# Kernel optimization log

Hardware: AMD Instinct MI355X
Metric: run time of the kernel (lower is better)

Reference implementation:

```python
import jax, jax.numpy as jnp
import numpy as np

# static config (matches init_kwargs / input_specs)
B, S, D, H, DH = 4, 2048, 2048, 16, 128
MAX_LEN = 1024  # round_up_to_multiple_of_256(max ragged length); lengths below max at 1024
ROPE_BASE = 10000.0


def setup_inputs() -> dict:
    key = jax.random.key(0)
    ks = jax.random.split(key, 8)
    q_src = jax.random.normal(ks[0], (B, MAX_LEN, D), jnp.float32)
    k_src = jax.random.normal(ks[1], (B, S, D), jnp.float32)
    v_src = jax.random.normal(ks[2], (B, S, D), jnp.float32)
    std = 1.0 / np.sqrt(D)
    Wq = jax.random.normal(ks[3], (D, H * DH), jnp.float32) * std
    Wk = jax.random.normal(ks[4], (D, H * DH), jnp.float32) * std
    Wv = jax.random.normal(ks[5], (D, H * DH), jnp.float32) * std
    Wo = jax.random.normal(ks[6], (H * DH, D), jnp.float32) * (1.0 / np.sqrt(H * DH))
    # mask[0]: causal bool [B,S,S]; mask[1]: full position ids [B,S]
    mask0 = jnp.broadcast_to(jnp.tril(jnp.ones((S, S), bool)), (B, S, S))
    pos_full = jnp.broadcast_to(jnp.arange(S, dtype=jnp.int32), (B, S))
    # ragged skip_mask: row i keeps lengths[i] random positions (max 1024 -> MAX_LEN)
    lengths = jnp.array([1024, 896, 768, 640], jnp.int32)
    scores = jax.random.uniform(ks[7], (B, S))
    ranks = jnp.argsort(jnp.argsort(scores, axis=1), axis=1)
    skip_mask = ranks < lengths[:, None]
    return {"q_src": q_src, "k_src": k_src, "v_src": v_src,
            "Wq": Wq, "Wk": Wk, "Wv": Wv, "Wo": Wo,
            "mask0": mask0, "pos_full": pos_full, "skip_mask": skip_mask}


def _rope(x, positions):
    # x: [B,H,L,DH], positions: [B,L] int -> rotary embedding on full head dim
    dh = x.shape[-1]
    inv_freq = 1.0 / (ROPE_BASE ** (jnp.arange(0, dh, 2, dtype=jnp.float32) / dh))
    freqs = positions.astype(jnp.float32)[:, :, None] * inv_freq      # [B,L,dh/2]
    emb = jnp.concatenate([freqs, freqs], axis=-1)[:, None]           # [B,1,L,dh]
    x1, x2 = jnp.split(x, 2, axis=-1)
    rot = jnp.concatenate([-x2, x1], axis=-1)                         # rotate_half
    return x * jnp.cos(emb) + rot * jnp.sin(emb)


def reference(q_src, k_src, v_src, Wq, Wk, Wv, Wo, mask0, pos_full, skip_mask):
    def heads(x, W):
        y = x @ W
        return y.reshape(x.shape[0], x.shape[1], H, DH).transpose(0, 2, 1, 3)

    q = heads(q_src, Wq)   # [B,H,MAX_LEN,DH]
    k = heads(k_src, Wk)   # [B,H,S,DH]
    v = heads(v_src, Wv)   # [B,H,S,DH]

    # _trim_attention_mask: gather kept rows (True-first, stable order), pad to MAX_LEN
    order = jnp.argsort(jnp.where(skip_mask, 0, 1), axis=1)[:, :MAX_LEN]  # [B,MAX_LEN]
    n = skip_mask.sum(axis=1)                                             # ragged lengths
    valid = jnp.arange(MAX_LEN)[None, :] < n[:, None]                     # [B,MAX_LEN]
    amask = jnp.take_along_axis(mask0, order[:, :, None], axis=1) & valid[:, :, None]
    pos_trim = jnp.where(valid, jnp.take_along_axis(pos_full, order, axis=1), 0)

    # RoPE: trimmed positions for q, full positions for k
    q = _rope(q, pos_trim)
    k = _rope(k, pos_full)

    # masked SDPA; fully-masked (padded) query rows -> zero output
    logits = jnp.einsum('bhld,bhsd->bhls', q, k) / np.sqrt(DH).astype(np.float32)
    logits = jnp.where(amask[:, None], logits, jnp.finfo(logits.dtype).min)
    probs = jax.nn.softmax(logits, axis=-1) * valid[:, None, :, None]
    ctx = jnp.einsum('bhls,bhsd->bhld', probs, v)                         # [B,H,MAX_LEN,DH]

    out = ctx.transpose(0, 2, 1, 3).reshape(B, MAX_LEN, H * DH) @ Wo     # [B,MAX_LEN,D]
    return out
```

## Files before the change

kernel.cpp:

```cpp
#include <hip/hip_runtime.h>

#define BB 4
#define SS 2048
#define DD 2048
#define HH 16
#define DHD 128
#define MAXL 1024

typedef __bf16 bf16x8 __attribute__((ext_vector_type(8)));
typedef float f32x4 __attribute__((ext_vector_type(4)));
typedef unsigned int u32_as1 __attribute__((address_space(1)));
typedef unsigned int u32_as3 __attribute__((address_space(3)));

__device__ __forceinline__ unsigned short f2bf(float f) {
  unsigned int u = __builtin_bit_cast(unsigned int, f);
  u += 0x7fffu + ((u >> 16) & 1u);
  return (unsigned short)(u >> 16);
}
__device__ __forceinline__ float bf2f(unsigned short h) {
  unsigned int u = ((unsigned int)h) << 16;
  return __builtin_bit_cast(float, u);
}
union U4 { uint4 u; bf16x8 b; };
__device__ __forceinline__ bf16x8 ldfrag(const unsigned short* p) {
  U4 x; x.u = *(const uint4*)p; return x.b;
}
__device__ __forceinline__ void gl_lds16(const void* g, void* l) {
  __builtin_amdgcn_global_load_lds((const u32_as1*)g, (u32_as3*)l, 16, 0, 0);
}

template <int C>
__device__ __forceinline__ float dppf(float x) {
  return __builtin_bit_cast(float,
      __builtin_amdgcn_mov_dpp(__builtin_bit_cast(int, x), C, 0xF, 0xF, true));
}
__device__ __forceinline__ float rmax16(float x) {
  x = fmaxf(x, dppf<0xB1>(x));
  x = fmaxf(x, dppf<0x4E>(x));
  x = fmaxf(x, dppf<0x141>(x));
  x = fmaxf(x, dppf<0x140>(x));
  return x;
}
__device__ __forceinline__ float radd16(float x) {
  x += dppf<0xB1>(x);
  x += dppf<0x4E>(x);
  x += dppf<0x141>(x);
  x += dppf<0x140>(x);
  return x;
}

__global__ void build_pos(const int* __restrict__ skip, int* __restrict__ posk,
                          int* __restrict__ nval) {
  int b = blockIdx.x, t = threadIdx.x;
  __shared__ int cnts[64], offs[64];
  const int* row = skip + b * SS;
  int c = 0;
  for (int i = 0; i < 32; i++) c += (row[t * 32 + i] != 0);
  cnts[t] = c;
  __syncthreads();
  if (t == 0) {
    int run = 0;
    for (int i = 0; i < 64; i++) { offs[i] = run; run += cnts[i]; }
    nval[b] = run > MAXL ? MAXL : run;
  }
  __syncthreads();
  int o = offs[t];
  for (int i = 0; i < 32; i++)
    if (row[t * 32 + i]) { if (o < MAXL) posk[b * MAXL + o] = t * 32 + i; o++; }
  int nb = nval[b];
  for (int l = nb + t; l < MAXL; l += 64) posk[b * MAXL + l] = -1;
}

__global__ __launch_bounds__(256) void cvt3(const float* __restrict__ q,
                                            const float* __restrict__ k,
                                            const float* __restrict__ v,
                                            unsigned short* __restrict__ oq,
                                            unsigned short* __restrict__ ok,
                                            unsigned short* __restrict__ ov) {
  const int nq = BB * MAXL * DD / 4, nk = BB * SS * DD / 4;
  int idx = blockIdx.x * 256 + threadIdx.x;
  const float* src; unsigned short* dst; int off;
  if (idx < nq) { src = q; dst = oq; off = idx; }
  else if (idx < nq + nk) { src = k; dst = ok; off = idx - nq; }
  else { src = v; dst = ov; off = idx - nq - nk; }
  float4 vv = ((const float4*)src)[off];
  ushort4 h;
  h.x = f2bf(vv.x); h.y = f2bf(vv.y); h.z = f2bf(vv.z); h.w = f2bf(vv.w);
  ((ushort4*)dst)[off] = h;
}

__global__ __launch_bounds__(256) void transpose_w4(const float* __restrict__ w0,
    const float* __restrict__ w1, const float* __restrict__ w2, const float* __restrict__ w3,
    unsigned short* __restrict__ o0, unsigned short* __restrict__ o1,
    unsigned short* __restrict__ o2, unsigned short* __restrict__ o3) {
  __shared__ __align__(16) unsigned short tile[64 * 76];
  const float* W; unsigned short* Wt;
  switch (blockIdx.z) {
    case 0: W = w0; Wt = o0; break;
    case 1: W = w1; Wt = o1; break;
    case 2: W = w2; Wt = o2; break;
    default: W = w3; Wt = o3; break;
  }
  int tx = threadIdx.x;
  int K0 = blockIdx.y * 64, N0 = blockIdx.x * 64;
  #pragma unroll
  for (int i = 0; i < 4; i++) {
    int r = (tx >> 4) + i * 16, c4 = (tx & 15) * 4;
    float4 v = *(const float4*)&W[(size_t)(K0 + r) * DD + N0 + c4];
    ushort4 h;
    h.x = f2bf(v.x); h.y = f2bf(v.y); h.z = f2bf(v.z); h.w = f2bf(v.w);
    *(ushort4*)&tile[r * 76 + c4] = h;
  }
  __syncthreads();
  #pragma unroll
  for (int i = 0; i < 4; i++) {
    int n = (tx >> 4) + i * 16, k4 = (tx & 15) * 4;
    ushort4 h;
    h.x = tile[(k4 + 0) * 76 + n];
    h.y = tile[(k4 + 1) * 76 + n];
    h.z = tile[(k4 + 2) * 76 + n];
    h.w = tile[(k4 + 3) * 76 + n];
    *(ushort4*)&Wt[(size_t)(N0 + n) * DD + K0 + k4] = h;
  }
}

template <int BM>
__global__ __launch_bounds__(512, 2) void gemm8(const unsigned short* __restrict__ A,
                                                const unsigned short* __restrict__ Bt,
                                                void* __restrict__ Cp,
                                                int M, int N, int K, int mode, int Lbits) {
  constexpr int AW = BM * 64;
  __shared__ __align__(16) unsigned short lds[(BM + 256) * 64 * 2];
  unsigned short* const Abuf = lds;
  unsigned short* const Bbuf = lds + 2 * AW;

  const int tid = threadIdx.x;
  const int lane = tid & 63, quad = lane >> 4, c = lane & 15;
  const int w = tid >> 6;
  const int wm = (w >> 2) * (BM / 2), wn = (w & 3) * 64;

  const int nwg = gridDim.x * gridDim.y;
  const int bid0 = blockIdx.y * gridDim.x + blockIdx.x;
  const int cpx = nwg >> 3;
  const int bid = (bid0 & 7) * cpx + (bid0 >> 3);
  const int bx = bid % gridDim.x;
  const int by = bid / gridDim.x;
  const size_t tm = (size_t)by * BM, tn = (size_t)bx * 256;

  constexpr int MR = BM / 32;
  f32x4 acc[MR][4] = {};

  const int trow = tid >> 3;
  const int tch = ((tid & 7) ^ (trow & 7)) * 8;
  const unsigned short* gA = A + (tm + trow) * (size_t)K + tch;
  const unsigned short* gB = Bt + (tn + trow) * (size_t)K + tch;
  constexpr int ALD = BM / 64;
  constexpr int NLD = ALD + 4;

  auto STAGE = [&](int sel, int kk) {
    unsigned short* ad = Abuf + sel * AW;
    unsigned short* bd = Bbuf + sel * 16384;
    #pragma unroll
    for (int i = 0; i < ALD; i++)
      gl_lds16(gA + kk + (size_t)(i * 64) * K, ad + i * 4096 + tid * 8);
    #pragma unroll
    for (int i = 0; i < 4; i++)
      gl_lds16(gB + kk + (size_t)(i * 64) * K, bd + i * 4096 + tid * 8);
  };

  const int nkt = K >> 6;
  STAGE(0, 0);

  for (int t = 0; t < nkt; ++t) {
    const int sel = t & 1;
    const unsigned short* as = Abuf + sel * AW;
    const unsigned short* bs = Bbuf + sel * 16384;
    if (t + 1 < nkt) {
      STAGE(sel ^ 1, (t + 1) << 6);
      asm volatile("s_waitcnt vmcnt(%0)" ::"i"(NLD) : "memory");
    } else {
      asm volatile("s_waitcnt vmcnt(0)" ::: "memory");
    }
    __builtin_amdgcn_s_barrier();

    bf16x8 a0[4][2], b01[2][2], b23[2][2];
    #pragma unroll
    for (int i = 0; i < 4; i++)
      #pragma unroll
      for (int ks = 0; ks < 2; ks++)
        a0[i][ks] = ldfrag(&as[(wm + i * 16 + c) * 64 + (((ks * 4 + quad) ^ (c & 7)) << 3)]);
    #pragma unroll
    for (int j = 0; j < 2; j++)
      #pragma unroll
      for (int ks = 0; ks < 2; ks++)
        b01[j][ks] = ldfrag(&bs[(wn + j * 16 + c) * 64 + (((ks * 4 + quad) ^ (c & 7)) << 3)]);
    __builtin_amdgcn_s_barrier();
    __builtin_amdgcn_s_setprio(1);
    #pragma unroll
    for (int i = 0; i < 4; i++)
      #pragma unroll
      for (int j = 0; j < 2; j++)
        #pragma unroll
        for (int ks = 0; ks < 2; ks++)
          acc[i][j] = __builtin_amdgcn_mfma_f32_16x16x32_bf16(a0[i][ks], b01[j][ks], acc[i][j], 0, 0, 0);
    __builtin_amdgcn_s_setprio(0);
    __builtin_amdgcn_s_barrier();
    #pragma unroll
    for (int j = 0; j < 2; j++)
      #pragma unroll
      for (int ks = 0; ks < 2; ks++)
        b23[j][ks] = ldfrag(&bs[(wn + 32 + j * 16 + c) * 64 + (((ks * 4 + quad) ^ (c & 7)) << 3)]);
    __builtin_amdgcn_s_barrier();
    __builtin_amdgcn_s_setprio(1);
    #pragma unroll
    for (int i = 0; i < 4; i++)
      #pragma unroll
      for (int j = 0; j < 2; j++)
        #pragma unroll
        for (int ks = 0; ks < 2; ks++)
          acc[i][2 + j] = __builtin_amdgcn_mfma_f32_16x16x32_bf16(a0[i][ks], b23[j][ks], acc[i][2 + j], 0, 0, 0);
    __builtin_amdgcn_s_setprio(0);
    __builtin_amdgcn_s_barrier();

    if constexpr (BM == 256) {
      bf16x8 a1[4][2];
      #pragma unroll
      for (int i = 0; i < 4; i++)
        #pragma unroll
        for (int ks = 0; ks < 2; ks++)
          a1[i][ks] = ldfrag(&as[(wm + 64 + i * 16 + c) * 64 + (((ks * 4 + quad) ^ (c & 7)) << 3)]);
      __builtin_amdgcn_s_barrier();
      __builtin_amdgcn_s_setprio(1);
      #pragma unroll
      for (int i = 0; i < 4; i++)
        #pragma unroll
        for (int j = 0; j < 2; j++)
          #pragma unroll
          for (int ks = 0; ks < 2; ks++)
            acc[4 + i][j] = __builtin_amdgcn_mfma_f32_16x16x32_bf16(a1[i][ks], b01[j][ks], acc[4 + i][j], 0, 0, 0);
      __builtin_amdgcn_s_setprio(0);
      __builtin_amdgcn_s_barrier();
      __builtin_amdgcn_s_setprio(1);
      #pragma unroll
      for (int i = 0; i < 4; i++)
        #pragma unroll
        for (int j = 0; j < 2; j++)
          #pragma unroll
          for (int ks = 0; ks < 2; ks++)
            acc[4 + i][2 + j] = __builtin_amdgcn_mfma_f32_16x16x32_bf16(a1[i][ks], b23[j][ks], acc[4 + i][2 + j], 0, 0, 0);
      __builtin_amdgcn_s_setprio(0);
      __builtin_amdgcn_s_barrier();
    }
  }

  if (mode == 1) {
    float* Cf = (float*)Cp;
    #pragma unroll
    for (int i = 0; i < MR; i++)
      #pragma unroll
      for (int j = 0; j < 4; j++)
        #pragma unroll
        for (int r = 0; r < 4; r++) {
          size_t m = tm + wm + i * 16 + quad * 4 + r;
          size_t n = tn + wn + j * 16 + c;
          Cf[m * N + n] = acc[i][j][r];
        }
    return;
  }
  unsigned short* Cb = (unsigned short*)Cp;
  unsigned short* ep = lds + w * 4352;
  constexpr int MH = BM / 128;
  if (mode == 0) {
    const size_t Lmask = ((size_t)1 << Lbits) - 1;
    #pragma unroll
    for (int mh = 0; mh < MH; mh++) {
      #pragma unroll
      for (int i = 0; i < 4; i++)
        #pragma unroll
        for (int j = 0; j < 4; j++)
          #pragma unroll
          for (int r = 0; r < 4; r++)
            ep[(i * 16 + quad * 4 + r) * 68 + j * 16 + c] = f2bf(acc[mh * 4 + i][j][r]);
      #pragma unroll
      for (int it = 0; it < 8; it++) {
        int chunk = it * 64 + lane;
        int ml = chunk >> 3, nc = (chunk & 7) * 8;
        uint4 val = *(const uint4*)&ep[ml * 68 + nc];
        size_t m = tm + wm + mh * 64 + ml, n = tn + wn + nc;
        size_t b = m >> Lbits, l = m & Lmask, h = n >> 7, d = n & 127;
        *(uint4*)&Cb[(((b * HH + h) << Lbits) + l) * 128 + d] = val;
      }
    }
  } else {
    #pragma unroll
    for (int mh = 0; mh < MH; mh++) {
      #pragma unroll
      for (int i = 0; i < 4; i++)
        #pragma unroll
        for (int j = 0; j < 4; j++)
          #pragma unroll
          for (int r = 0; r < 4; r++)
            ep[(j * 16 + c) * 68 + i * 16 + quad * 4 + r] = f2bf(acc[mh * 4 + i][j][r]);
      #pragma unroll
      for (int it = 0; it < 8; it++) {
        int chunk = it * 64 + lane;
        int nl = chunk >> 3, mc = (chunk & 7) * 8;
        uint4 val = *(const uint4*)&ep[nl * 68 + mc];
        size_t n = tn + wn + nl, m = tm + wm + mh * 64 + mc;
        size_t b = m >> 11, s = m & 2047, h = n >> 7, d = n & 127;
        *(uint4*)&Cb[((b * HH + h) * 128 + d) * SS + s] = val;
      }
    }
  }
}

__global__ __launch_bounds__(256) void rope2(unsigned short* __restrict__ xq,
                                             unsigned short* __restrict__ xk,
                                             const int* __restrict__ posk) {
  const int Nq = BB * HH * MAXL * 64;
  int gid = blockIdx.x * 256 + threadIdx.x;
  unsigned short* x; int Lbits, idx, use_posk;
  if (gid < Nq) { x = xq; Lbits = 10; use_posk = 1; idx = gid; }
  else { x = xk; Lbits = 11; use_posk = 0; idx = gid - Nq; }
  int d = idx & 63;
  int rest = idx >> 6;
  int l = rest & ((1 << Lbits) - 1);
  int bh = rest >> Lbits;
  int b = bh >> 4;
  int p = use_posk ? posk[(b << 10) + l] : l;
  float ang = (float)p * __expf(-(float)d * 0.14391156831212787f);
  float sn, cs;
  __sincosf(ang, &sn, &cs);
  size_t base = (size_t)rest * 128;
  float x1 = bf2f(x[base + d]), x2 = bf2f(x[base + d + 64]);
  x[base + d]      = f2bf(x1 * cs - x2 * sn);
  x[base + d + 64] = f2bf(x2 * cs + x1 * sn);
}

__global__ __launch_bounds__(256) void attn_kernel(const unsigned short* __restrict__ qp,
                                                   const unsigned short* __restrict__ kp,
                                                   const unsigned short* __restrict__ vtp,
                                                   const int* __restrict__ posk,
                                                   const int* __restrict__ nval,
                                                   unsigned short* __restrict__ ctx) {
  __shared__ __align__(16) unsigned short k_s[2][64 * 128];
  __shared__ __align__(16) unsigned short vt_s[2][128 * 64];
  __shared__ __align__(16) unsigned short p_s[4 * 16 * 72];
  __shared__ int km_s[64];

  const int tid = threadIdx.x;
  const int w = tid >> 6, lane = tid & 63, quad = lane >> 4, c = lane & 15;
  const int bh = blockIdx.x, b = bh >> 4, h = bh & 15;
  const int qbase = blockIdx.y * 64;
  const int nb = nval[b];

  if (tid < 64) {
    int l = qbase + tid;
    km_s[tid] = (l < nb) ? posk[(b << 10) + l] : -1;
  }
  __syncthreads();

  const unsigned short* qg = qp + (((size_t)bh << 10) + qbase) * 128;
  bf16x8 aq[4];
  #pragma unroll
  for (int ks = 0; ks < 4; ks++)
    aq[ks] = ldfrag(&qg[(size_t)(w * 16 + c) * 128 + ks * 32 + quad * 8]);

  int lv = nb - 1 - qbase; lv = lv > 63 ? 63 : lv;
  const int tile_kmax = (lv >= 0) ? km_s[lv] : -1;
  const int nkt = (tile_kmax >= 0) ? ((tile_kmax >> 6) + 1) : 0;

  int wl = w * 16 + 15; if (wl > lv) wl = lv;
  const int wkmax = (wl >= w * 16) ? km_s[wl] : -1;

  int km[4];
  #pragma unroll
  for (int r = 0; r < 4; r++) km[r] = km_s[w * 16 + quad * 4 + r];

  const int srow = tid >> 4;
  const int kswz = (tid & 15) ^ (srow & 7);
  const unsigned short* kgp = kp + ((size_t)bh << 11) * 128 + (size_t)srow * 128 + kswz * 8;
  const int dvrow = tid >> 3;
  const int vswz = (tid & 7) ^ (dvrow & 7);
  const unsigned short* vgp = vtp + ((size_t)bh * 128 + dvrow) * SS + vswz * 8;

  auto STG = [&](int buf, int kb) {
    #pragma unroll
    for (int i = 0; i < 4; i++)
      gl_lds16(kgp + ((size_t)kb + i * 16) * 128, &k_s[buf][(i * 256 + tid) * 8]);
    #pragma unroll
    for (int i = 0; i < 4; i++)
      gl_lds16(vgp + (size_t)kb + (size_t)i * 32 * SS, &vt_s[buf][(i * 256 + tid) * 8]);
  };

  float m_i[4], l_i[4];
  #pragma unroll
  for (int r = 0; r < 4; r++) { m_i[r] = -1e30f; l_i[r] = 0.f; }
  f32x4 o[8];
  #pragma unroll
  for (int dj = 0; dj < 8; dj++) o[dj] = (f32x4){0.f, 0.f, 0.f, 0.f};

  if (nkt > 0) STG(0, 0);

  for (int kt = 0; kt < nkt; kt++) {
    const int cur = kt & 1;
    const int kb = kt * 64;
    if (kt + 1 < nkt) {
      STG(cur ^ 1, kb + 64);
      asm volatile("s_waitcnt vmcnt(8)" ::: "memory");
    } else {
      asm volatile("s_waitcnt vmcnt(0)" ::: "memory");
    }
    __builtin_amdgcn_s_barrier();

    if (kb <= wkmax) {
      f32x4 sa[4];
      #pragma unroll
      for (int j = 0; j < 4; j++) {
        sa[j] = (f32x4){0.f, 0.f, 0.f, 0.f};
        #pragma unroll
        for (int ks = 0; ks < 4; ks++) {
          bf16x8 bk = ldfrag(&k_s[cur][((j * 16 + c) << 7) + (((ks * 4 + quad) ^ (c & 7)) << 3)]);
          sa[j] = __builtin_amdgcn_mfma_f32_16x16x32_bf16(aq[ks], bk, sa[j], 0, 0, 0);
        }
      }

      const float scale = 0.08838834764831843f;
      float mt[4] = {-1e30f, -1e30f, -1e30f, -1e30f};
      #pragma unroll
      for (int j = 0; j < 4; j++) {
        int key = kb + j * 16 + c;
        #pragma unroll
        for (int r = 0; r < 4; r++) {
          float v = (key <= km[r]) ? sa[j][r] * scale : -1e30f;
          sa[j][r] = v;
          mt[r] = fmaxf(mt[r], v);
        }
      }
      float al[4], rs[4];
      #pragma unroll
      for (int r = 0; r < 4; r++) {
        mt[r] = rmax16(mt[r]);
        float mn = fmaxf(m_i[r], mt[r]);
        al[r] = __expf(m_i[r] - mn);
        m_i[r] = mn;
        rs[r] = 0.f;
      }
      #pragma unroll
      for (int j = 0; j < 4; j++)
        #pragma unroll
        for (int r = 0; r < 4; r++) {
          float pv = __expf(sa[j][r] - m_i[r]);
          sa[j][r] = pv;
          rs[r] += pv;
        }
      #pragma unroll
      for (int r = 0; r < 4; r++) {
        rs[r] = radd16(rs[r]);
        l_i[r] = l_i[r] * al[r] + rs[r];
      }
      #pragma unroll
      for (int dj = 0; dj < 8; dj++)
        #pragma unroll
        for (int r = 0; r < 4; r++) o[dj][r] *= al[r];

      #pragma unroll
      for (int j = 0; j < 4; j++)
        #pragma unroll
        for (int r = 0; r < 4; r++)
          p_s[w * 1152 + (quad * 4 + r) * 72 + j * 16 + c] = f2bf(sa[j][r]);

      #pragma unroll
      for (int ks2 = 0; ks2 < 2; ks2++) {
        bf16x8 ap = ldfrag(&p_s[w * 1152 + c * 72 + ks2 * 32 + quad * 8]);
        #pragma unroll
        for (int dj = 0; dj < 8; dj++) {
          bf16x8 bv = ldfrag(&vt_s[cur][((dj * 16 + c) << 6) + (((ks2 * 4 + quad) ^ (c & 7)) << 3)]);
          o[dj] = __builtin_amdgcn_mfma_f32_16x16x32_bf16(ap, bv, o[dj], 0, 0, 0);
        }
      }
    }
    __builtin_amdgcn_s_barrier();
  }

  #pragma unroll
  for (int r = 0; r < 4; r++) {
    int l = qbase + w * 16 + quad * 4 + r;
    bool ok = (l < nb);
    float inv = ok ? (1.0f / l_i[r]) : 0.0f;
    #pragma unroll
    for (int dj = 0; dj < 8; dj++)
      ctx[(((size_t)b << 10) + l) * (size_t)DD + h * 128 + dj * 16 + c] =
          f2bf(ok ? o[dj][r] * inv : 0.0f);
  }
}

extern "C" void kernel_launch(void* const* d_in, const int* in_sizes, int n_in,
                              void* d_out, int out_size, void* d_ws, size_t ws_size,
                              hipStream_t stream) {
  const float* q_src = (const float*)d_in[0];
  const float* k_src = (const float*)d_in[1];
  const float* v_src = (const float*)d_in[2];
  const float* Wq = (const float*)d_in[3];
  const float* Wk = (const float*)d_in[4];
  const float* Wv = (const float*)d_in[5];
  const float* Wo = (const float*)d_in[6];
  const int* skip = (const int*)d_in[9];

  char* p = (char*)d_ws;
  auto alloc = [&](size_t bytes) -> char* {
    char* r = p;
    p += (bytes + 255) & ~(size_t)255;
    return r;
  };
  unsigned short* a_q  = (unsigned short*)alloc((size_t)BB * MAXL * DD * 2);
  unsigned short* a_k  = (unsigned short*)alloc((size_t)BB * SS * DD * 2);
  unsigned short* a_v  = (unsigned short*)alloc((size_t)BB * SS * DD * 2);
  unsigned short* wt_q = (unsigned short*)alloc((size_t)DD * DD * 2);
  unsigned short* wt_k = (unsigned short*)alloc((size_t)DD * DD * 2);
  unsigned short* wt_v = (unsigned short*)alloc((size_t)DD * DD * 2);
  unsigned short* wt_o = (unsigned short*)alloc((size_t)DD * DD * 2);
  unsigned short* q_pro = (unsigned short*)alloc((size_t)BB * HH * MAXL * DHD * 2);
  unsigned short* k_pro = (unsigned short*)alloc((size_t)BB * HH * SS * DHD * 2);
  unsigned short* v_t   = (unsigned short*)alloc((size_t)BB * HH * SS * DHD * 2);
  int* posk = (int*)alloc((size_t)BB * MAXL * 4);
  int* nval = (int*)alloc(64);
  unsigned short* ctx = a_q;

  build_pos<<<BB, 64, 0, stream>>>(skip, posk, nval);
  cvt3<<<(BB * MAXL * DD + 2 * BB * SS * DD) / (4 * 256), 256, 0, stream>>>(
      q_src, k_src, v_src, a_q, a_k, a_v);
  transpose_w4<<<dim3(32, 32, 4), 256, 0, stream>>>(Wq, Wk, Wv, Wo, wt_q, wt_k, wt_v, wt_o);

  gemm8<128><<<dim3(8, 32), 512, 0, stream>>>(a_q, wt_q, q_pro, BB * MAXL, DD, DD, 0, 10);
  gemm8<256><<<dim3(8, 32), 512, 0, stream>>>(a_k, wt_k, k_pro, BB * SS, DD, DD, 0, 11);
  gemm8<256><<<dim3(8, 32), 512, 0, stream>>>(a_v, wt_v, v_t, BB * SS, DD, DD, 2, 11);

  rope2<<<(BB * HH * (MAXL + SS) * 64) / 256, 256, 0, stream>>>(q_pro, k_pro, posk);

  attn_kernel<<<dim3(BB * HH, MAXL / 64), 256, 0, stream>>>(q_pro, k_pro, v_t, posk, nval, ctx);

  gemm8<128><<<dim3(8, 32), 512, 0, stream>>>(ctx, wt_o, d_out, BB * MAXL, DD, DD, 1, 0);
}
```

Measured before the change: 692.7 us.

## Use fragment-major LDS layout, split K/V staging, fold scale and log2e into Q

The GEMM and attention kernels now store tiles in LDS in a fragment-major order, so each lane reads its MFMA fragment at lane*8 with no XOR swizzle arithmetic. The attention kernel moves from double-buffered K/V to single buffers with separate K and V prefetches placed between compute phases. This cuts LDS use, and launch bounds now request 4 blocks per CU. The softmax scale and log2e are folded into Q during RoPE so exp2 can be used directly. Masking is skipped for tiles that lie entirely below the causal limit. Single buffering with extra barriers may expose load latency, and the bf16 rounding of the prescaled Q changes slightly.

```diff
diff --git a/kernel.cpp b/kernel.cpp
--- a/kernel.cpp
+++ b/kernel.cpp
@@ -129,10 +129,10 @@
                                                 const unsigned short* __restrict__ Bt,
                                                 void* __restrict__ Cp,
                                                 int M, int N, int K, int mode, int Lbits) {
-  constexpr int AW = BM * 64;
-  __shared__ __align__(16) unsigned short lds[(BM + 256) * 64 * 2];
+  constexpr int AFR = BM / 8;
+  __shared__ __align__(16) unsigned short lds[(AFR + 32) * 1024];
   unsigned short* const Abuf = lds;
-  unsigned short* const Bbuf = lds + 2 * AW;
+  unsigned short* const Bbuf = lds + 2 * AFR * 512;
 
   const int tid = threadIdx.x;
   const int lane = tid & 63, quad = lane >> 4, c = lane & 15;
@@ -150,31 +150,36 @@
   constexpr int MR = BM / 32;
   f32x4 acc[MR][4] = {};
 
-  const int trow = tid >> 3;
-  const int tch = ((tid & 7) ^ (trow & 7)) * 8;
-  const unsigned short* gA = A + (tm + trow) * (size_t)K + tch;
-  const unsigned short* gB = Bt + (tn + trow) * (size_t)K + tch;
-  constexpr int ALD = BM / 64;
-  constexpr int NLD = ALD + 4;
+  constexpr int AN = AFR / 8;
+  constexpr int NLD = AN + 4;
+  const unsigned short* gA = A + (tm + c) * (size_t)K + quad * 8;
+  const unsigned short* gB = Bt + (tn + c) * (size_t)K + quad * 8;
 
   auto STAGE = [&](int sel, int kk) {
-    unsigned short* ad = Abuf + sel * AW;
-    unsigned short* bd = Bbuf + sel * 16384;
-    #pragma unroll
-    for (int i = 0; i < ALD; i++)
-      gl_lds16(gA + kk + (size_t)(i * 64) * K, ad + i * 4096 + tid * 8);
-    #pragma unroll
-    for (int i = 0; i < 4; i++)
-      gl_lds16(gB + kk + (size_t)(i * 64) * K, bd + i * 4096 + tid * 8);
+    unsigned short* ad = Abuf + sel * (AFR * 512) + lane * 8;
+    unsigned short* bd = Bbuf + sel * 16384 + lane * 8;
+    #pragma unroll
+    for (int n = 0; n < AN; n++) {
+      int f = n * 8 + w;
+      gl_lds16(gA + kk + ((size_t)(f >> 1) * 16) * K + (f & 1) * 32, ad + f * 512);
+    }
+    #pragma unroll
+    for (int n = 0; n < 4; n++) {
+      int f = n * 8 + w;
+      gl_lds16(gB + kk + ((size_t)(f >> 1) * 16) * K + (f & 1) * 32, bd + f * 512);
+    }
   };
 
   const int nkt = K >> 6;
   STAGE(0, 0);
 
+  const int ai0 = (wm >> 4) * 2;
+  const int bj0 = (wn >> 4) * 2;
+
   for (int t = 0; t < nkt; ++t) {
     const int sel = t & 1;
-    const unsigned short* as = Abuf + sel * AW;
-    const unsigned short* bs = Bbuf + sel * 16384;
+    const unsigned short* as = Abuf + sel * (AFR * 512) + lane * 8;
+    const unsigned short* bs = Bbuf + sel * 16384 + lane * 8;
     if (t + 1 < nkt) {
       STAGE(sel ^ 1, (t + 1) << 6);
       asm volatile("s_waitcnt vmcnt(%0)" ::"i"(NLD) : "memory");
@@ -188,12 +193,12 @@
     for (int i = 0; i < 4; i++)
       #pragma unroll
       for (int ks = 0; ks < 2; ks++)
-        a0[i][ks] = ldfrag(&as[(wm + i * 16 + c) * 64 + (((ks * 4 + quad) ^ (c & 7)) << 3)]);
+        a0[i][ks] = ldfrag(&as[(ai0 + i * 2 + ks) * 512]);
     #pragma unroll
     for (int j = 0; j < 2; j++)
       #pragma unroll
       for (int ks = 0; ks < 2; ks++)
-        b01[j][ks] = ldfrag(&bs[(wn + j * 16 + c) * 64 + (((ks * 4 + quad) ^ (c & 7)) << 3)]);
+        b01[j][ks] = ldfrag(&bs[(bj0 + j * 2 + ks) * 512]);
     __builtin_amdgcn_s_barrier();
     __builtin_amdgcn_s_setprio(1);
     #pragma unroll
@@ -209,7 +214,7 @@
     for (int j = 0; j < 2; j++)
       #pragma unroll
       for (int ks = 0; ks < 2; ks++)
-        b23[j][ks] = ldfrag(&bs[(wn + 32 + j * 16 + c) * 64 + (((ks * 4 + quad) ^ (c & 7)) << 3)]);
+        b23[j][ks] = ldfrag(&bs[(bj0 + (2 + j) * 2 + ks) * 512]);
     __builtin_amdgcn_s_barrier();
     __builtin_amdgcn_s_setprio(1);
     #pragma unroll
@@ -228,7 +233,7 @@
       for (int i = 0; i < 4; i++)
         #pragma unroll
         for (int ks = 0; ks < 2; ks++)
-          a1[i][ks] = ldfrag(&as[(wm + 64 + i * 16 + c) * 64 + (((ks * 4 + quad) ^ (c & 7)) << 3)]);
+          a1[i][ks] = ldfrag(&as[(ai0 + (4 + i) * 2 + ks) * 512]);
       __builtin_amdgcn_s_barrier();
       __builtin_amdgcn_s_setprio(1);
       #pragma unroll
@@ -317,6 +322,7 @@
 __global__ __launch_bounds__(256) void rope2(unsigned short* __restrict__ xq,
                                              unsigned short* __restrict__ xk,
                                              const int* __restrict__ posk) {
+  constexpr float QSCL = (float)(0.08838834764831843 * 1.4426950408889634);
   const int Nq = BB * HH * MAXL * 64;
   int gid = blockIdx.x * 256 + threadIdx.x;
   unsigned short* x; int Lbits, idx, use_posk;
@@ -331,34 +337,40 @@
   float ang = (float)p * __expf(-(float)d * 0.14391156831212787f);
   float sn, cs;
   __sincosf(ang, &sn, &cs);
+  float S = use_posk ? QSCL : 1.0f;
   size_t base = (size_t)rest * 128;
   float x1 = bf2f(x[base + d]), x2 = bf2f(x[base + d + 64]);
-  x[base + d]      = f2bf(x1 * cs - x2 * sn);
-  x[base + d + 64] = f2bf(x2 * cs + x1 * sn);
-}
-
-__global__ __launch_bounds__(256) void attn_kernel(const unsigned short* __restrict__ qp,
-                                                   const unsigned short* __restrict__ kp,
-                                                   const unsigned short* __restrict__ vtp,
-                                                   const int* __restrict__ posk,
-                                                   const int* __restrict__ nval,
-                                                   unsigned short* __restrict__ ctx) {
-  __shared__ __align__(16) unsigned short k_s[2][64 * 128];
-  __shared__ __align__(16) unsigned short vt_s[2][128 * 64];
-  __shared__ __align__(16) unsigned short p_s[4 * 16 * 72];
-  __shared__ int km_s[64];
+  x[base + d]      = f2bf((x1 * cs - x2 * sn) * S);
+  x[base + d + 64] = f2bf((x2 * cs + x1 * sn) * S);
+}
+
+__global__ __launch_bounds__(256, 4) void attn_kernel(const unsigned short* __restrict__ qp,
+                                                      const unsigned short* __restrict__ kp,
+                                                      const unsigned short* __restrict__ vtp,
+                                                      const int* __restrict__ posk,
+                                                      const int* __restrict__ nval,
+                                                      unsigned short* __restrict__ ctx) {
+  __shared__ __align__(16) unsigned short k_s[8192];
+  __shared__ __align__(16) unsigned short vt_s[8192];
+  __shared__ __align__(16) unsigned short p_s[4096];
 
   const int tid = threadIdx.x;
   const int w = tid >> 6, lane = tid & 63, quad = lane >> 4, c = lane & 15;
   const int bh = blockIdx.x, b = bh >> 4, h = bh & 15;
   const int qbase = blockIdx.y * 64;
   const int nb = nval[b];
-
-  if (tid < 64) {
-    int l = qbase + tid;
-    km_s[tid] = (l < nb) ? posk[(b << 10) + l] : -1;
-  }
-  __syncthreads();
+  const int* pb = posk + (b << 10) + qbase;
+
+  int lv = nb - 1 - qbase; lv = lv > 63 ? 63 : lv;
+  const int nkt = (lv >= 0) ? ((pb[lv] >> 6) + 1) : 0;
+  const bool whas = (w * 16 <= lv);
+  int wl = w * 16 + 15; if (wl > lv) wl = lv;
+  const int wkmax = whas ? pb[wl] : -1;
+  const int kminw = whas ? pb[w * 16] : -1;
+
+  int km[4];
+  #pragma unroll
+  for (int r = 0; r < 4; r++) km[r] = pb[w * 16 + quad * 4 + r];
 
   const unsigned short* qg = qp + (((size_t)bh << 10) + qbase) * 128;
   bf16x8 aq[4];
@@ -366,31 +378,19 @@
   for (int ks = 0; ks < 4; ks++)
     aq[ks] = ldfrag(&qg[(size_t)(w * 16 + c) * 128 + ks * 32 + quad * 8]);
 
-  int lv = nb - 1 - qbase; lv = lv > 63 ? 63 : lv;
-  const int tile_kmax = (lv >= 0) ? km_s[lv] : -1;
-  const int nkt = (tile_kmax >= 0) ? ((tile_kmax >> 6) + 1) : 0;
-
-  int wl = w * 16 + 15; if (wl > lv) wl = lv;
-  const int wkmax = (wl >= w * 16) ? km_s[wl] : -1;
-
-  int km[4];
-  #pragma unroll
-  for (int r = 0; r < 4; r++) km[r] = km_s[w * 16 + quad * 4 + r];
-
-  const int srow = tid >> 4;
-  const int kswz = (tid & 15) ^ (srow & 7);
-  const unsigned short* kgp = kp + ((size_t)bh << 11) * 128 + (size_t)srow * 128 + kswz * 8;
-  const int dvrow = tid >> 3;
-  const int vswz = (tid & 7) ^ (dvrow & 7);
-  const unsigned short* vgp = vtp + ((size_t)bh * 128 + dvrow) * SS + vswz * 8;
-
-  auto STG = [&](int buf, int kb) {
-    #pragma unroll
-    for (int i = 0; i < 4; i++)
-      gl_lds16(kgp + ((size_t)kb + i * 16) * 128, &k_s[buf][(i * 256 + tid) * 8]);
-    #pragma unroll
-    for (int i = 0; i < 4; i++)
-      gl_lds16(vgp + (size_t)kb + (size_t)i * 32 * SS, &vt_s[buf][(i * 256 + tid) * 8]);
+  const unsigned short* kgp = kp + ((size_t)bh * SS + c) * 128 + (w * 4 + quad) * 8;
+  auto STG_K = [&](int kb) {
+    #pragma unroll
+    for (int n = 0; n < 4; n++)
+      gl_lds16(kgp + (size_t)(kb + n * 16) * 128, &k_s[(n * 4 + w) * 512 + lane * 8]);
+  };
+  auto STG_V = [&](int kb) {
+    #pragma unroll
+    for (int n = 0; n < 4; n++) {
+      int f = n * 4 + w;
+      gl_lds16(vtp + ((size_t)bh * 128 + (f >> 1) * 16 + c) * SS + kb + ((f & 1) * 4 + quad) * 8,
+               &vt_s[f * 512 + lane * 8]);
+    }
   };
 
   float m_i[4], l_i[4];
@@ -400,41 +400,49 @@
   #pragma unroll
   for (int dj = 0; dj < 8; dj++) o[dj] = (f32x4){0.f, 0.f, 0.f, 0.f};
 
-  if (nkt > 0) STG(0, 0);
+  const int pwb = w * 1024 + quad * 32 + (c & 7) + (c >> 3) * 128;
+
+  if (nkt > 0) { STG_K(0); STG_V(0); }
 
   for (int kt = 0; kt < nkt; kt++) {
-    const int cur = kt & 1;
     const int kb = kt * 64;
-    if (kt + 1 < nkt) {
-      STG(cur ^ 1, kb + 64);
-      asm volatile("s_waitcnt vmcnt(8)" ::: "memory");
-    } else {
-      asm volatile("s_waitcnt vmcnt(0)" ::: "memory");
-    }
-    __builtin_amdgcn_s_barrier();
-
-    if (kb <= wkmax) {
-      f32x4 sa[4];
+    const bool more = (kt + 1 < nkt);
+    asm volatile("s_waitcnt vmcnt(8)" ::: "memory");
+    __builtin_amdgcn_s_barrier();
+
+    const bool act = (kb <= wkmax);
+    f32x4 sa[4];
+    if (act) {
       #pragma unroll
       for (int j = 0; j < 4; j++) {
         sa[j] = (f32x4){0.f, 0.f, 0.f, 0.f};
         #pragma unroll
         for (int ks = 0; ks < 4; ks++) {
-          bf16x8 bk = ldfrag(&k_s[cur][((j * 16 + c) << 7) + (((ks * 4 + quad) ^ (c & 7)) << 3)]);
+          bf16x8 bk = ldfrag(&k_s[(j * 4 + ks) * 512 + lane * 8]);
           sa[j] = __builtin_amdgcn_mfma_f32_16x16x32_bf16(aq[ks], bk, sa[j], 0, 0, 0);
         }
       }
-
-      const float scale = 0.08838834764831843f;
+    }
+    __builtin_amdgcn_s_barrier();
+    if (more) STG_K(kb + 64);
+
+    if (act) {
       float mt[4] = {-1e30f, -1e30f, -1e30f, -1e30f};
-      #pragma unroll
-      for (int j = 0; j < 4; j++) {
-        int key = kb + j * 16 + c;
-        #pragma unroll
-        for (int r = 0; r < 4; r++) {
-          float v = (key <= km[r]) ? sa[j][r] * scale : -1e30f;
-          sa[j][r] = v;
-          mt[r] = fmaxf(mt[r], v);
+      if (kb + 63 <= kminw) {
+        #pragma unroll
+        for (int j = 0; j < 4; j++)
+          #pragma unroll
+          for (int r = 0; r < 4; r++) mt[r] = fmaxf(mt[r], sa[j][r]);
+      } else {
+        #pragma unroll
+        for (int j = 0; j < 4; j++) {
+          int key = kb + j * 16 + c;
+          #pragma unroll
+          for (int r = 0; r < 4; r++) {
+            float v = (key <= km[r]) ? sa[j][r] : -1e30f;
+            sa[j][r] = v;
+            mt[r] = fmaxf(mt[r], v);
+          }
         }
       }
       float al[4], rs[4];
@@ -442,7 +450,7 @@
       for (int r = 0; r < 4; r++) {
         mt[r] = rmax16(mt[r]);
         float mn = fmaxf(m_i[r], mt[r]);
-        al[r] = __expf(m_i[r] - mn);
+        al[r] = __builtin_exp2f(m_i[r] - mn);
         m_i[r] = mn;
         rs[r] = 0.f;
       }
@@ -450,7 +458,7 @@
       for (int j = 0; j < 4; j++)
         #pragma unroll
         for (int r = 0; r < 4; r++) {
-          float pv = __expf(sa[j][r] - m_i[r]);
+          float pv = __builtin_exp2f(sa[j][r] - m_i[r]);
           sa[j][r] = pv;
           rs[r] += pv;
         }
@@ -463,24 +471,30 @@
       for (int dj = 0; dj < 8; dj++)
         #pragma unroll
         for (int r = 0; r < 4; r++) o[dj][r] *= al[r];
-
+    }
+
+    if (more) { asm volatile("s_waitcnt vmcnt(8)" ::: "memory"); }
+    else      { asm volatile("s_waitcnt vmcnt(0)" ::: "memory"); }
+    __builtin_amdgcn_s_barrier();
+
+    if (act) {
       #pragma unroll
       for (int j = 0; j < 4; j++)
         #pragma unroll
         for (int r = 0; r < 4; r++)
-          p_s[w * 1152 + (quad * 4 + r) * 72 + j * 16 + c] = f2bf(sa[j][r]);
-
+          p_s[pwb + (j >> 1) * 512 + (j & 1) * 256 + r * 8] = f2bf(sa[j][r]);
       #pragma unroll
       for (int ks2 = 0; ks2 < 2; ks2++) {
-        bf16x8 ap = ldfrag(&p_s[w * 1152 + c * 72 + ks2 * 32 + quad * 8]);
+        bf16x8 ap = ldfrag(&p_s[(w * 2 + ks2) * 512 + lane * 8]);
         #pragma unroll
         for (int dj = 0; dj < 8; dj++) {
-          bf16x8 bv = ldfrag(&vt_s[cur][((dj * 16 + c) << 6) + (((ks2 * 4 + quad) ^ (c & 7)) << 3)]);
+          bf16x8 bv = ldfrag(&vt_s[(dj * 2 + ks2) * 512 + lane * 8]);
           o[dj] = __builtin_amdgcn_mfma_f32_16x16x32_bf16(ap, bv, o[dj], 0, 0, 0);
         }
       }
     }
     __builtin_amdgcn_s_barrier();
+    if (more) STG_V(kb + 64);
   }
 
   #pragma unroll
```

New measurement: 809.3 us. 1.17x slower.
